# Kernel optimization log

Measured on AMD Instinct MI355X. Metric: run time of the kernel, lower is better.

## Reference

```python
import jax, jax.numpy as jnp
import numpy as np

B, S, D = 2, 2048, 4096
N_HEADS, N_KV_HEADS = 32, 8
HEAD_DIM = D // N_HEADS  # 128
N_REP = N_HEADS // N_KV_HEADS
NEG_INF = -1e9  # finite stand-in for -inf additive causal mask


def apply_rotary_emb(x, freqs_cis):
    # x: [b, s, h, hd]; freqs_cis: [s, hd//2, 2] (cos, sin)
    b, s, h, hd = x.shape
    xr = x.reshape(b, s, h, hd // 2, 2)
    fc = freqs_cis.reshape(1, s, 1, hd // 2, 2)
    o0 = xr[..., 0] * fc[..., 0] - xr[..., 1] * fc[..., 1]
    o1 = xr[..., 1] * fc[..., 0] + xr[..., 0] * fc[..., 1]
    return jnp.stack([o0, o1], axis=-1).reshape(b, s, h, hd)


def setup_inputs() -> dict:
    key = jax.random.key(0)
    ks = jax.random.split(key, 6)
    x = jax.random.normal(ks[0], (B, S, D), dtype=jnp.float32)
    # weights stored torch-style: [out_features, in_features]
    wq = jax.random.normal(ks[1], (N_HEADS * HEAD_DIM, D), dtype=jnp.float32) * 0.02
    wk = jax.random.normal(ks[2], (N_KV_HEADS * HEAD_DIM, D), dtype=jnp.float32) * 0.02
    wv = jax.random.normal(ks[3], (N_KV_HEADS * HEAD_DIM, D), dtype=jnp.float32) * 0.02
    wo = jax.random.normal(ks[4], (D, N_HEADS * HEAD_DIM), dtype=jnp.float32) * 0.02
    # rotary table (Llama-style, theta=10000)
    inv_freq = 1.0 / (10000.0 ** (np.arange(0, HEAD_DIM, 2, dtype=np.float32) / HEAD_DIM))
    angles = np.arange(S, dtype=np.float32)[:, None] * inv_freq[None, :]
    freqs_cis = jnp.asarray(np.stack([np.cos(angles), np.sin(angles)], axis=-1))  # [S, hd//2, 2]
    # additive causal mask
    mask = jnp.where(jnp.tril(jnp.ones((S, S), dtype=bool)), 0.0, NEG_INF).astype(jnp.float32)
    return {"x": x, "start_pos": 0, "freqs_cis": freqs_cis, "mask": mask,
            "wq": wq, "wk": wk, "wv": wv, "wo": wo}


def reference(x, start_pos, freqs_cis, mask, wq, wk, wv, wo):
    b, s, _ = x.shape
    xq = jnp.einsum('bsd,ed->bse', x, wq).reshape(b, s, N_HEADS, HEAD_DIM)
    xk = jnp.einsum('bsd,ed->bse', x, wk).reshape(b, s, N_KV_HEADS, HEAD_DIM)
    xv = jnp.einsum('bsd,ed->bse', x, wv).reshape(b, s, N_KV_HEADS, HEAD_DIM)
    xq = apply_rotary_emb(xq, freqs_cis)
    xk = apply_rotary_emb(xk, freqs_cis)
    # repeat_kv (repeat_interleave along head dim)
    xk = jnp.repeat(xk, N_REP, axis=2)
    xv = jnp.repeat(xv, N_REP, axis=2)
    q = xq.transpose(0, 2, 1, 3)  # [b, h, s, hd]
    k = xk.transpose(0, 2, 1, 3)
    v = xv.transpose(0, 2, 1, 3)
    scores = jnp.einsum('bhqd,bhkd->bhqk', q, k) / jnp.sqrt(jnp.float32(HEAD_DIM))
    scores = scores + mask[None, None, :, :]
    probs = jax.nn.softmax(scores.astype(jnp.float32), axis=-1).astype(q.dtype)
    out = jnp.einsum('bhqk,bhkd->bhqd', probs, v)
    out = out.transpose(0, 2, 1, 3).reshape(b, s, N_HEADS * HEAD_DIM)
    return jnp.einsum('bse,de->bsd', out, wo)
```

## Files before the change

kernel.cpp:

```cpp
#include <hip/hip_runtime.h>
#include <cstdint>
#include <cstddef>

#define B_   2
#define S_   2048
#define D_   4096
#define H_   32
#define KVH_ 8
#define HD_  128

typedef unsigned short u16;
typedef short     bf16x8 __attribute__((ext_vector_type(8)));
typedef float     f32x4  __attribute__((ext_vector_type(4)));
typedef float     f32x16 __attribute__((ext_vector_type(16)));
typedef u16       u16x8  __attribute__((ext_vector_type(8)));
typedef uint32_t  u32x2  __attribute__((ext_vector_type(2)));
typedef uint32_t  u32x4  __attribute__((ext_vector_type(4)));

__device__ __forceinline__ u16 f2bf(float f) {
  union { float f; uint32_t u; } v; v.f = f;
  uint32_t u = v.u;
  return (u16)((u + 0x7fffu + ((u >> 16) & 1u)) >> 16);
}
__device__ __forceinline__ float bf2f(u16 h) {
  union { uint32_t u; float f; } v; v.u = ((uint32_t)h) << 16;
  return v.f;
}
__device__ __forceinline__ uint32_t cvtpk(float lo, float hi_) {
  uint32_t r; asm("v_cvt_pk_bf16_f32 %0, %1, %2" : "=v"(r) : "v"(lo), "v"(hi_)); return r;
}
__device__ __forceinline__ float exp2v(float x) {
  float r; asm("v_exp_f32 %0, %1" : "=v"(r) : "v"(x)); return r;
}

__device__ __forceinline__ void gl_lds16(const void* g, void* l) {
  __builtin_amdgcn_global_load_lds(
      (const __attribute__((address_space(1))) void*)g,
      (__attribute__((address_space(3))) void*)l, 16, 0, 0);
}

#define MFMA(a, b, c)  __builtin_amdgcn_mfma_f32_16x16x32_bf16((a), (b), (c), 0, 0, 0)
#define MFMA32(a, b, c) __builtin_amdgcn_mfma_f32_32x32x16_bf16((a), (b), (c), 0, 0, 0)
#define PLSWAP(x, y) asm volatile("v_permlane32_swap_b32 %0, %1" : "+v"(x), "+v"(y))

__global__ void cast_kernel(const float* __restrict__ in, u16* __restrict__ out, int n8) {
  int i = blockIdx.x * blockDim.x + threadIdx.x;
  if (i >= n8) return;
  const float4* p = (const float4*)in + (size_t)i * 2;
  float4 a = p[0], b = p[1];
  u16x8 r;
  r[0] = f2bf(a.x); r[1] = f2bf(a.y); r[2] = f2bf(a.z); r[3] = f2bf(a.w);
  r[4] = f2bf(b.x); r[5] = f2bf(b.y); r[6] = f2bf(b.z); r[7] = f2bf(b.w);
  *((u16x8*)out + i) = r;
}

template <bool OUT_F32>
__global__ __launch_bounds__(256, 2)
void gemm_bt(const u16* __restrict__ A, const u16* __restrict__ Bw,
             void* __restrict__ C, int M, int N, int K) {
  __shared__ u16 lA[128 * 32];
  __shared__ u16 lB[128 * 32];
  const int tid = threadIdx.x;
  const int w = tid >> 6, l = tid & 63;
  const int lc = l & 15, lg = l >> 4;
  const int bn = blockIdx.x, bm = blockIdx.y;
  const int wr = w >> 1, wc = w & 1;
  const u16* Ab = A + (size_t)(bm * 128) * K;
  const u16* Bb = Bw + (size_t)(bn * 128) * K;
  const int srow = l >> 2;
  const int scol = (l & 3) * 8;

  f32x4 acc[4][4];
#pragma unroll
  for (int i = 0; i < 4; ++i)
#pragma unroll
    for (int j = 0; j < 4; ++j) acc[i][j] = (f32x4){0.f, 0.f, 0.f, 0.f};

  const int nk = K >> 5;
  for (int kt = 0; kt < nk; ++kt) {
    const int k0 = kt * 32;
    __syncthreads();
#pragma unroll
    for (int i = 0; i < 2; ++i) {
      const int rowA = (w * 2 + i) * 16;
      gl_lds16(Ab + (size_t)(rowA + srow) * K + k0 + scol, &lA[rowA * 32]);
      gl_lds16(Bb + (size_t)(rowA + srow) * K + k0 + scol, &lB[rowA * 32]);
    }
    __syncthreads();
    bf16x8 af[4], bfr[4];
#pragma unroll
    for (int mi = 0; mi < 4; ++mi)
      af[mi] = *(const bf16x8*)&lA[(wr * 64 + mi * 16 + lc) * 32 + lg * 8];
#pragma unroll
    for (int ni = 0; ni < 4; ++ni)
      bfr[ni] = *(const bf16x8*)&lB[(wc * 64 + ni * 16 + lc) * 32 + lg * 8];
#pragma unroll
    for (int mi = 0; mi < 4; ++mi)
#pragma unroll
      for (int ni = 0; ni < 4; ++ni)
        acc[mi][ni] = MFMA(af[mi], bfr[ni], acc[mi][ni]);
  }

#pragma unroll
  for (int mi = 0; mi < 4; ++mi)
#pragma unroll
    for (int ni = 0; ni < 4; ++ni)
#pragma unroll
      for (int r = 0; r < 4; ++r) {
        const int row = bm * 128 + wr * 64 + mi * 16 + lg * 4 + r;
        const int col = bn * 128 + wc * 64 + ni * 16 + lc;
        if constexpr (OUT_F32)
          ((float*)C)[(size_t)row * N + col] = acc[mi][ni][r];
        else
          ((u16*)C)[(size_t)row * N + col] = f2bf(acc[mi][ni][r]);
      }
}

template <bool OUT_F32>
__global__ __launch_bounds__(512, 2)
void gemm256_bt(const u16* __restrict__ A, const u16* __restrict__ Bw,
                void* __restrict__ C, int M, int N, int K) {
  __shared__ u16 sA[2 * 256 * 64];
  __shared__ u16 sB[2 * 256 * 64];
  const int tid = threadIdx.x;
  const int w = tid >> 6, l = tid & 63;
  const int lc = l & 15, lg = l >> 4;
  const int wm = w >> 2, wn = w & 3;
  const int nbn = N >> 8;
  const int nwg = (M >> 8) * nbn;
  const int cpx = nwg >> 3;
  const int lin = blockIdx.x;
  const int swz = (lin & 7) * cpx + (lin >> 3);
  const int bm = swz / nbn, bn = swz % nbn;
  const u16* Ab = A + (size_t)(bm * 256) * K;
  const u16* Bb = Bw + (size_t)(bn * 256) * K;
  const int lr = l >> 3;
  const int scc = ((l & 7) ^ lr) * 8;
  int cxg[2];
#pragma unroll
  for (int kk = 0; kk < 2; ++kk) cxg[kk] = ((kk * 4 + lg) ^ (lc & 7)) * 8;

  f32x4 acc[8][4];
#pragma unroll
  for (int i = 0; i < 8; ++i)
#pragma unroll
    for (int j = 0; j < 4; ++j) acc[i][j] = (f32x4){0.f, 0.f, 0.f, 0.f};

  auto STAGEA = [&](int buf, int t1, int h) {
    const int k0 = t1 * 64;
#pragma unroll
    for (int j = 0; j < 2; ++j) {
      const int r0 = h * 128 + w * 16 + j * 8;
      gl_lds16(Ab + (size_t)(r0 + lr) * K + k0 + scc, &sA[buf * 16384 + r0 * 64]);
    }
  };
  auto STAGEB = [&](int buf, int t1, int h) {
    const int k0 = t1 * 64;
#pragma unroll
    for (int j = 0; j < 2; ++j) {
      const int r0 = h * 128 + w * 16 + j * 8;
      gl_lds16(Bb + (size_t)(r0 + lr) * K + k0 + scc, &sB[buf * 16384 + r0 * 64]);
    }
  };

  const int nk = K >> 6;
  STAGEA(0, 0, 0); STAGEB(0, 0, 0);
  STAGEB(0, 0, 1); STAGEA(0, 0, 1);
  if (nk > 1) { STAGEA(1, 1, 0); STAGEB(1, 1, 0); }

  for (int t = 0; t < nk; ++t) {
    const int cur = t & 1;
    const int cb = cur * 16384;
    const int nb = (cur ^ 1);
#pragma unroll
    for (int p = 0; p < 4; ++p) {
      const int ha = p >> 1, hb = p & 1;
      if (p == 0)      asm volatile("s_waitcnt vmcnt(8)" ::: "memory");
      else if (p == 1) asm volatile("s_waitcnt vmcnt(10)" ::: "memory");
      else if (p == 2) asm volatile("s_waitcnt vmcnt(8)" ::: "memory");
      __builtin_amdgcn_s_barrier();
      asm volatile("" ::: "memory");
      bf16x8 af[4][2], bfr[2][2];
#pragma unroll
      for (int mi = 0; mi < 4; ++mi)
#pragma unroll
        for (int kk = 0; kk < 2; ++kk)
          af[mi][kk] = *(const bf16x8*)
              &sA[cb + (ha * 128 + wm * 64 + mi * 16 + lc) * 64 + cxg[kk]];
#pragma unroll
      for (int ni = 0; ni < 2; ++ni)
#pragma unroll
        for (int kk = 0; kk < 2; ++kk)
          bfr[ni][kk] = *(const bf16x8*)
              &sB[cb + (hb * 128 + wn * 32 + ni * 16 + lc) * 64 + cxg[kk]];
      if (p == 0 && t + 1 < nk) { STAGEB(nb, t + 1, 1); STAGEA(nb, t + 1, 1); }
      if (p == 2 && t + 2 < nk) { STAGEA(cur, t + 2, 0); }
      if (p == 3 && t + 2 < nk) { STAGEB(cur, t + 2, 0); }
      asm volatile("s_waitcnt lgkmcnt(0)" ::: "memory");
      __builtin_amdgcn_sched_barrier(0);
      __builtin_amdgcn_s_setprio(1);
#pragma unroll
      for (int kk = 0; kk < 2; ++kk)
#pragma unroll
        for (int mi = 0; mi < 4; ++mi)
#pragma unroll
          for (int ni = 0; ni < 2; ++ni)
            acc[ha * 4 + mi][hb * 2 + ni] =
                MFMA(af[mi][kk], bfr[ni][kk], acc[ha * 4 + mi][hb * 2 + ni]);
      __builtin_amdgcn_s_setprio(0);
    }
  }

#pragma unroll
  for (int ha = 0; ha < 2; ++ha)
#pragma unroll
    for (int mi = 0; mi < 4; ++mi)
#pragma unroll
      for (int hb = 0; hb < 2; ++hb)
#pragma unroll
        for (int ni = 0; ni < 2; ++ni)
#pragma unroll
          for (int r = 0; r < 4; ++r) {
            const int row = bm * 256 + ha * 128 + wm * 64 + mi * 16 + lg * 4 + r;
            const int col = bn * 256 + hb * 128 + wn * 32 + ni * 16 + lc;
            if constexpr (OUT_F32)
              ((float*)C)[(size_t)row * N + col] = acc[ha * 4 + mi][hb * 2 + ni][r];
            else
              ((u16*)C)[(size_t)row * N + col] = f2bf(acc[ha * 4 + mi][hb * 2 + ni][r]);
          }
}

template <int NH, int STRIDE, int OFF>
__global__ void rope_kernel(const u16* __restrict__ lin, const float* __restrict__ fr,
                            u16* __restrict__ out, float scale) {
  int idx = blockIdx.x * 256 + threadIdx.x;
  const int total = B_ * S_ * NH * 64;
  if (idx >= total) return;
  const int i = idx & 63;
  const int h = (idx >> 6) % NH;
  const int t = idx / (64 * NH);
  const int s = t & (S_ - 1);
  const int b = t >> 11;
  const size_t src = (size_t)t * STRIDE + OFF + h * HD_ + 2 * i;
  const float x0 = bf2f(lin[src]);
  const float x1 = bf2f(lin[src + 1]);
  const float2 cs = ((const float2*)fr)[s * 64 + i];
  const float o0 = (x0 * cs.x - x1 * cs.y) * scale;
  const float o1 = (x1 * cs.x + x0 * cs.y) * scale;
  const size_t dst = ((size_t)((b * NH + h) * S_ + s)) * HD_ + 2 * i;
  out[dst] = f2bf(o0);
  out[dst + 1] = f2bf(o1);
}

__global__ void vtrans_kernel(const u16* __restrict__ kvlin, u16* __restrict__ vt) {
  __shared__ u16 tile[32][33];
  const int tx = threadIdx.x, ty = threadIdx.y;
  const int s0 = blockIdx.x * 32;
  const int d0 = blockIdx.y * 32;
  const int bk = blockIdx.z;
  const int b = bk >> 3, kv = bk & 7;
#pragma unroll
  for (int r = 0; r < 4; ++r) {
    const int s = s0 + ty + r * 8;
    tile[ty + r * 8][tx] =
        kvlin[((size_t)(b * S_ + s)) * 2048 + 1024 + kv * HD_ + d0 + tx];
  }
  __syncthreads();
#pragma unroll
  for (int r = 0; r < 4; ++r) {
    const int d = d0 + ty + r * 8;
    vt[((size_t)bk * HD_ + d) * S_ + s0 + tx] = tile[tx][ty + r * 8];
  }
}

__global__ __launch_bounds__(256, 2)
void attn_kernel(const u16* __restrict__ Q, const u16* __restrict__ K,
                 const u16* __restrict__ V, u16* __restrict__ O) {
  __shared__ u16 sK[2][64 * HD_];
  __shared__ u16 sV[2][HD_ * 64];
  const int tid = threadIdx.x;
  const int w = tid >> 6, l = tid & 63;
  const int hi = l >> 5, q32 = l & 31;
  const int kv = blockIdx.y, b = blockIdx.z;
  const int h = kv * 4 + w;
  const u16* Kp = K + ((size_t)(b * KVH_ + kv) * S_) * HD_;
  const u16* Vp = V + ((size_t)(b * KVH_ + kv) * HD_) * S_;

  int koff[4], voff[4];
#pragma unroll
  for (int i = 0; i < 4; ++i) {
    const int kr = w * 16 + i * 4 + (l >> 4);
    koff[i] = kr * HD_ + (((l & 15) ^ (kr & 7))) * 8;
    const int vr = w * 32 + i * 8 + (l >> 3);
    voff[i] = vr * S_ + (((l & 7) ^ (vr & 7))) * 8;
  }
  int cx[8];
#pragma unroll
  for (int c = 0; c < 8; ++c) cx[c] = ((c * 2 + hi) ^ (l & 7)) * 8;

  auto STAGE = [&](int bufi, int ti) {
    const u16* kg = Kp + (size_t)ti * (64 * HD_);
    const u16* vg = Vp + (size_t)ti * 64;
#pragma unroll
    for (int i = 0; i < 4; ++i) {
      gl_lds16(kg + koff[i], &sK[bufi][(w * 16 + i * 4) * HD_]);
      gl_lds16(vg + voff[i], &sV[bufi][(w * 32 + i * 8) * 64]);
    }
  };

  int cur = 0;
  for (int seg = 0; seg < 2; ++seg) {
    const int qt = seg ? (63 - blockIdx.x) : blockIdx.x;
    const int qg = qt * 32 + q32;
    const u16* Qp = Q + ((size_t)(b * H_ + h) * S_ + qt * 32) * HD_;

    bf16x8 qf[8];
#pragma unroll
    for (int ds = 0; ds < 8; ++ds)
      qf[ds] = *(const bf16x8*)(Qp + (size_t)q32 * HD_ + ds * 16 + hi * 8);
    asm volatile("s_waitcnt vmcnt(0)" ::: "memory");

    f32x16 out[4];
#pragma unroll
    for (int d = 0; d < 4; ++d)
#pragma unroll
      for (int r = 0; r < 16; ++r) out[d][r] = 0.f;
    float mrun = -1e30f, lrun = 0.f;

    const int nt = (qt >> 1) + 1;
    STAGE(cur, 0);

    for (int t = 0; t < nt; ++t) {
      if (t + 1 < nt) {
        STAGE(cur ^ 1, t + 1);
        asm volatile("s_waitcnt vmcnt(8)" ::: "memory");
      } else {
        asm volatile("s_waitcnt vmcnt(0)" ::: "memory");
      }
      __builtin_amdgcn_s_barrier();
      asm volatile("" ::: "memory");

      f32x16 sc0, sc1;
#pragma unroll
      for (int r = 0; r < 16; ++r) { sc0[r] = 0.f; sc1[r] = 0.f; }
      __builtin_amdgcn_s_setprio(1);
#pragma unroll
      for (int ds = 0; ds < 8; ++ds) {
        bf16x8 kf0 = *(const bf16x8*)&sK[cur][q32 * HD_ + cx[ds]];
        bf16x8 kf1 = *(const bf16x8*)&sK[cur][(32 + q32) * HD_ + cx[ds]];
        sc0 = MFMA32(kf0, qf[ds], sc0);
        sc1 = MFMA32(kf1, qf[ds], sc1);
      }
      __builtin_amdgcn_s_setprio(0);

      const bool diag = (t == nt - 1);
      float p0[16], p1[16];
#pragma unroll
      for (int r = 0; r < 16; ++r) {
        const int krow = (r & 3) + 8 * (r >> 2) + 4 * hi;
        float v0 = sc0[r], v1 = sc1[r];
        if (diag) {
          if (t * 64 + krow > qg) v0 = -1e9f;
          if (t * 64 + 32 + krow > qg) v1 = -1e9f;
        }
        p0[r] = v0; p1[r] = v1;
      }
      float rm = -1e30f;
#pragma unroll
      for (int r = 0; r < 16; ++r) rm = fmaxf(rm, fmaxf(p0[r], p1[r]));
      rm = fmaxf(rm, __shfl_xor(rm, 32, 64));
      if (!__all(rm <= mrun + 8.0f)) {
        const float mnew = fmaxf(mrun, rm);
        const float alpha = exp2v(mrun - mnew);
        mrun = mnew;
        lrun *= alpha;
#pragma unroll
        for (int d = 0; d < 4; ++d) out[d] *= alpha;
      }
      float sum = 0.f;
#pragma unroll
      for (int r = 0; r < 16; ++r) {
        p0[r] = exp2v(p0[r] - mrun);
        p1[r] = exp2v(p1[r] - mrun);
        sum += p0[r] + p1[r];
      }
      sum += __shfl_xor(sum, 32, 64);
      lrun += sum;
      uint32_t pk0[8], pk1[8];
#pragma unroll
      for (int g = 0; g < 4; ++g) {
        pk0[2 * g]     = cvtpk(p0[4 * g], p0[4 * g + 1]);
        pk0[2 * g + 1] = cvtpk(p0[4 * g + 2], p0[4 * g + 3]);
        pk1[2 * g]     = cvtpk(p1[4 * g], p1[4 * g + 1]);
        pk1[2 * g + 1] = cvtpk(p1[4 * g + 2], p1[4 * g + 3]);
      }
      PLSWAP(pk0[0], pk0[2]); PLSWAP(pk0[1], pk0[3]);
      PLSWAP(pk0[4], pk0[6]); PLSWAP(pk0[5], pk0[7]);
      PLSWAP(pk1[0], pk1[2]); PLSWAP(pk1[1], pk1[3]);
      PLSWAP(pk1[4], pk1[6]); PLSWAP(pk1[5], pk1[7]);
      bf16x8 pa[4];
      pa[0] = __builtin_bit_cast(bf16x8, (u32x4){pk0[0], pk0[1], pk0[2], pk0[3]});
      pa[1] = __builtin_bit_cast(bf16x8, (u32x4){pk0[4], pk0[5], pk0[6], pk0[7]});
      pa[2] = __builtin_bit_cast(bf16x8, (u32x4){pk1[0], pk1[1], pk1[2], pk1[3]});
      pa[3] = __builtin_bit_cast(bf16x8, (u32x4){pk1[4], pk1[5], pk1[6], pk1[7]});
      __builtin_amdgcn_s_setprio(1);
#pragma unroll
      for (int d = 0; d < 4; ++d) {
        const int vbase = (d * 32 + q32) * 64;
#pragma unroll
        for (int kk = 0; kk < 4; ++kk) {
          bf16x8 vf = *(const bf16x8*)&sV[cur][vbase + cx[kk]];
          out[d] = MFMA32(vf, pa[kk], out[d]);
        }
      }
      __builtin_amdgcn_s_setprio(0);
      asm volatile("" ::: "memory");
      __builtin_amdgcn_s_barrier();
      cur ^= 1;
    }

    const float inv = 1.0f / lrun;
    u16* myS = ((u16*)sK) + w * 4096;
#pragma unroll
    for (int d = 0; d < 4; ++d)
#pragma unroll
      for (int rq = 0; rq < 4; ++rq) {
        u32x2 pw;
        pw[0] = cvtpk(out[d][rq * 4 + 0] * inv, out[d][rq * 4 + 1] * inv);
        pw[1] = cvtpk(out[d][rq * 4 + 2] * inv, out[d][rq * 4 + 3] * inv);
        const int gin = (d * 8 + rq * 2 + hi) ^ (q32 & 15);
        *(u32x2*)&myS[q32 * 128 + gin * 4] = pw;
      }
    asm volatile("s_waitcnt lgkmcnt(0)" ::: "memory");
    __builtin_amdgcn_sched_barrier(0);
    const int rr = l >> 4;
    const int cc = l & 15;
#pragma unroll
    for (int p = 0; p < 8; ++p) {
      const int q = p * 4 + rr;
      const int ga = (2 * cc) ^ (q & 15);
      const int gb = (2 * cc + 1) ^ (q & 15);
      u32x2 va = *(const u32x2*)&myS[q * 128 + ga * 4];
      u32x2 vb = *(const u32x2*)&myS[q * 128 + gb * 4];
      u32x4 val = {va[0], va[1], vb[0], vb[1]};
      *(u32x4*)&O[((size_t)(b * S_ + qt * 32 + q)) * (H_ * HD_) + h * HD_ + cc * 8] = val;
    }
    if (seg == 0) {
      asm volatile("" ::: "memory");
      __builtin_amdgcn_s_barrier();
    }
  }
}

extern "C" void kernel_launch(void* const* d_in, const int* in_sizes, int n_in,
                              void* d_out, int out_size, void* d_ws, size_t ws_size,
                              hipStream_t stream) {
  const float* x     = (const float*)d_in[0];
  const float* freqs = (const float*)d_in[2];
  const float* wq    = (const float*)d_in[4];
  const float* wk    = (const float*)d_in[5];
  const float* wv    = (const float*)d_in[6];
  const float* wo    = (const float*)d_in[7];

  char* ws = (char*)d_ws;
  u16* xb    = (u16*)(ws + 0);
  u16* wqb   = (u16*)(ws + 33554432);
  u16* wkb   = (u16*)(ws + 67108864);
  u16* wvb   = (u16*)(ws + 75497472);
  u16* qlin  = (u16*)(ws + 83886080);
  u16* kvlin = (u16*)(ws + 117440512);
  u16* qr   = wqb;
  u16* kr   = wkb;
  u16* vt   = wvb;
  u16* aout = qlin;
  u16* wob  = xb;

  cast_kernel<<<8192, 256, 0, stream>>>(x, xb, 2097152);
  cast_kernel<<<8192, 256, 0, stream>>>(wq, wqb, 2097152);
  cast_kernel<<<2048, 256, 0, stream>>>(wk, wkb, 524288);
  cast_kernel<<<2048, 256, 0, stream>>>(wv, wvb, 524288);
  gemm256_bt<false><<<256, 512, 0, stream>>>(xb, wqb, qlin, 4096, 4096, 4096);
  gemm_bt<false><<<dim3(16, 32), 256, 0, stream>>>(xb, wkb, kvlin, 4096, 2048, 4096);
  rope_kernel<32, 4096, 0><<<32768, 256, 0, stream>>>(qlin, freqs, qr,
      0.08838834764831845f * 1.4426950408889634f);
  rope_kernel<8, 2048, 0><<<8192, 256, 0, stream>>>(kvlin, freqs, kr, 1.0f);
  vtrans_kernel<<<dim3(64, 4, 16), dim3(32, 8), 0, stream>>>(kvlin, vt);
  attn_kernel<<<dim3(32, 8, 2), 256, 0, stream>>>(qr, kr, vt, aout);
  cast_kernel<<<8192, 256, 0, stream>>>(wo, wob, 2097152);
  gemm256_bt<true><<<256, 512, 0, stream>>>(aout, wob, d_out, 4096, 4096, 4096);
}
```

Baseline: 527.1 us.

## Software-pipeline LDS fragment loads behind MFMAs and reuse B fragments across quadrants

Restructures the GEMM inner loop so LDS fragment reads for the next quadrant are issued right after the current quadrant's MFMAs, overlapping LDS latency with matrix math. The quadrant order becomes (0,0),(0,1),(1,1),(1,0), so A and B fragments stay in registers and are reused instead of being reloaded for every quadrant. The vmcnt wait counts are hand-tuned per phase. This needs more live registers and relies on fragile waitcnt and barrier accounting. The nk>1 guard on the prologue prefetch is removed.

```diff
diff --git a/kernel.cpp b/kernel.cpp
--- a/kernel.cpp
+++ b/kernel.cpp
@@ -163,53 +163,87 @@
     }
   };
 
+  bf16x8 afr[4][2], b0r[2][2], b1r[2][2];
+  auto LDA = [&](int base, int ha) {
+#pragma unroll
+    for (int mi = 0; mi < 4; ++mi)
+#pragma unroll
+      for (int kk = 0; kk < 2; ++kk)
+        afr[mi][kk] = *(const bf16x8*)
+            &sA[base + (ha * 128 + wm * 64 + mi * 16 + lc) * 64 + cxg[kk]];
+  };
+  auto LDB0 = [&](int base) {
+#pragma unroll
+    for (int ni = 0; ni < 2; ++ni)
+#pragma unroll
+      for (int kk = 0; kk < 2; ++kk)
+        b0r[ni][kk] = *(const bf16x8*)
+            &sB[base + (wn * 32 + ni * 16 + lc) * 64 + cxg[kk]];
+  };
+  auto LDB1 = [&](int base) {
+#pragma unroll
+    for (int ni = 0; ni < 2; ++ni)
+#pragma unroll
+      for (int kk = 0; kk < 2; ++kk)
+        b1r[ni][kk] = *(const bf16x8*)
+            &sB[base + (128 + wn * 32 + ni * 16 + lc) * 64 + cxg[kk]];
+  };
+
+#define VMW(N_) asm volatile("s_waitcnt vmcnt(" #N_ ")" ::: "memory")
+#define BARR do { __builtin_amdgcn_s_barrier(); asm volatile("" ::: "memory"); } while (0)
+#define LGKM do { asm volatile("s_waitcnt lgkmcnt(0)" ::: "memory"); \
+                  __builtin_amdgcn_sched_barrier(0); } while (0)
+#define MMQ(HA, HB, BF) do { __builtin_amdgcn_s_setprio(1); \
+  _Pragma("unroll") for (int kk = 0; kk < 2; ++kk) \
+  _Pragma("unroll") for (int mi = 0; mi < 4; ++mi) \
+  _Pragma("unroll") for (int ni = 0; ni < 2; ++ni) \
+    acc[(HA) * 4 + mi][(HB) * 2 + ni] = \
+        MFMA(afr[mi][kk], BF[ni][kk], acc[(HA) * 4 + mi][(HB) * 2 + ni]); \
+  __builtin_amdgcn_s_setprio(0); } while (0)
+
   const int nk = K >> 6;
   STAGEA(0, 0, 0); STAGEB(0, 0, 0);
   STAGEB(0, 0, 1); STAGEA(0, 0, 1);
-  if (nk > 1) { STAGEA(1, 1, 0); STAGEB(1, 1, 0); }
+  STAGEA(1, 1, 0); STAGEB(1, 1, 0);
+  VMW(8);
+  BARR;
+  LDA(0, 0); LDB0(0);
 
   for (int t = 0; t < nk; ++t) {
     const int cur = t & 1;
     const int cb = cur * 16384;
-    const int nb = (cur ^ 1);
-#pragma unroll
-    for (int p = 0; p < 4; ++p) {
-      const int ha = p >> 1, hb = p & 1;
-      if (p == 0)      asm volatile("s_waitcnt vmcnt(8)" ::: "memory");
-      else if (p == 1) asm volatile("s_waitcnt vmcnt(10)" ::: "memory");
-      else if (p == 2) asm volatile("s_waitcnt vmcnt(8)" ::: "memory");
-      __builtin_amdgcn_s_barrier();
-      asm volatile("" ::: "memory");
-      bf16x8 af[4][2], bfr[2][2];
-#pragma unroll
-      for (int mi = 0; mi < 4; ++mi)
-#pragma unroll
-        for (int kk = 0; kk < 2; ++kk)
-          af[mi][kk] = *(const bf16x8*)
-              &sA[cb + (ha * 128 + wm * 64 + mi * 16 + lc) * 64 + cxg[kk]];
-#pragma unroll
-      for (int ni = 0; ni < 2; ++ni)
-#pragma unroll
-        for (int kk = 0; kk < 2; ++kk)
-          bfr[ni][kk] = *(const bf16x8*)
-              &sB[cb + (hb * 128 + wn * 32 + ni * 16 + lc) * 64 + cxg[kk]];
-      if (p == 0 && t + 1 < nk) { STAGEB(nb, t + 1, 1); STAGEA(nb, t + 1, 1); }
-      if (p == 2 && t + 2 < nk) { STAGEA(cur, t + 2, 0); }
-      if (p == 3 && t + 2 < nk) { STAGEB(cur, t + 2, 0); }
-      asm volatile("s_waitcnt lgkmcnt(0)" ::: "memory");
-      __builtin_amdgcn_sched_barrier(0);
-      __builtin_amdgcn_s_setprio(1);
-#pragma unroll
-      for (int kk = 0; kk < 2; ++kk)
-#pragma unroll
-        for (int mi = 0; mi < 4; ++mi)
-#pragma unroll
-          for (int ni = 0; ni < 2; ++ni)
-            acc[ha * 4 + mi][hb * 2 + ni] =
-                MFMA(af[mi][kk], bfr[ni][kk], acc[ha * 4 + mi][hb * 2 + ni]);
-      __builtin_amdgcn_s_setprio(0);
-    }
+    const int nbb = (cur ^ 1) * 16384;
+    const bool n1 = (t + 1 < nk), n2 = (t + 2 < nk);
+
+    if (n1) VMW(6); else VMW(2);
+    BARR;
+    if (n1) { STAGEB(cur ^ 1, t + 1, 1); STAGEA(cur ^ 1, t + 1, 1); }
+    LGKM;
+    MMQ(0, 0, b0r);
+    LDB1(cb);
+
+    if (n1) VMW(8); else VMW(0);
+    BARR;
+    LGKM;
+    MMQ(0, 1, b1r);
+    LDA(cb, 1);
+
+    BARR;
+    if (n2) STAGEA(cur, t + 2, 0);
+    LGKM;
+    MMQ(1, 1, b1r);
+
+    if (n1) { if (n2) VMW(6); else VMW(4); }
+    BARR;
+    if (n2) STAGEB(cur, t + 2, 0);
+    LGKM;
+    MMQ(1, 0, b0r);
+    if (n1) { LDA(nbb, 0); LDB0(nbb); }
   }
+#undef VMW
+#undef BARR
+#undef LGKM
+#undef MMQ
 
 #pragma unroll
   for (int ha = 0; ha < 2; ++ha)
```

After: 546.9 us. 3.8% more time.
